# Performance work log

Measured on AMD Instinct MI355X. Metric: run time of the kernel, lower is better.

Reference implementation:

```python
import jax, jax.numpy as jnp
import numpy as np

MARGIN = 0.3
EPS = 1e-6  # torch pairwise_distance default eps used by TripletMarginLoss


def setup_inputs() -> dict:
    key = jax.random.key(0)
    k1, k2 = jax.random.split(key)
    emb = jax.random.normal(k1, (4096, 256), dtype=jnp.float32)
    emb = emb / jnp.linalg.norm(emb, axis=1, keepdims=True)  # docstring: normalized embeddings
    labels = jax.random.randint(k2, (4096,), 0, 64, dtype=jnp.int64) if jax.config.jax_enable_x64 else jax.random.randint(k2, (4096,), 0, 64, dtype=jnp.int32)
    return {"embeddings": emb, "labels": labels}


def _triplet_mining_loss(embeddings, labels):
    B = embeddings.shape[0]
    # pairwise euclidean distances via GEMM (matches torch.cdist p=2)
    sq = jnp.sum(embeddings * embeddings, axis=1)
    d2 = sq[:, None] + sq[None, :] - 2.0 * (embeddings @ embeddings.T)
    dist = jnp.sqrt(jnp.maximum(d2, 0.0))  # [B, B]

    same = labels[:, None] == labels[None, :]
    eye = jnp.eye(B, dtype=bool)
    pos_mask = same & ~eye
    neg_mask = ~same
    valid = pos_mask.any(axis=1) & neg_mask.any(axis=1)

    # hardest positive per anchor
    ap = jnp.where(pos_mask, dist, -jnp.inf)
    hp_idx = jnp.argmax(ap, axis=1)                           # [B]
    ap_dist = jnp.take_along_axis(dist, hp_idx[:, None], 1)[:, 0]

    # semi-hard negative: ap < d_an < ap + margin; pick FIRST such index (original takes semi_hard_indices[0])
    semi = neg_mask & (dist > ap_dist[:, None]) & (dist < ap_dist[:, None] + MARGIN)
    any_semi = semi.any(axis=1)
    first_semi = jnp.argmax(semi, axis=1)                     # argmax of bool = first True
    an = jnp.where(neg_mask, dist, jnp.inf)
    hardest_neg = jnp.argmin(an, axis=1)
    neg_idx = jnp.where(any_semi, first_semi, hardest_neg)

    # triplet margin loss recomputed from embeddings (torch adds EPS inside the norm)
    pos_e = embeddings[hp_idx]
    neg_e = embeddings[neg_idx]
    d_ap = jnp.linalg.norm(embeddings - pos_e + EPS, axis=1)
    d_an = jnp.linalg.norm(embeddings - neg_e + EPS, axis=1)
    per_anchor = jnp.maximum(d_ap - d_an + MARGIN, 0.0)

    vf = valid.astype(embeddings.dtype)
    cnt = jnp.sum(vf)
    return jnp.where(cnt > 0, jnp.sum(per_anchor * vf) / jnp.maximum(cnt, 1.0), 0.0)


def reference(embeddings, labels):
    return _triplet_mining_loss(embeddings, labels)
```

## Files before the change

### kernel.cpp

```cpp
#include <hip/hip_runtime.h>
#include <math.h>

#define BN 4096
#define DIM 256
#define D4 (DIM/4)
#define MI 8
#define MT 16
#define MARGINF 0.3f
#define EPSF 1e-6f
#define SCAP 96
#define IMAX 0x7fffffff

typedef __attribute__((ext_vector_type(8))) short bf16x8;
typedef __attribute__((ext_vector_type(4))) float f32x4;

__device__ __forceinline__ float fma4(float4 a, float4 b, float c){
  return fmaf(a.x,b.x, fmaf(a.y,b.y, fmaf(a.z,b.z, fmaf(a.w,b.w, c))));
}
__device__ __forceinline__ unsigned short f2bf(float x){
  unsigned u = __float_as_uint(x);
  return (unsigned short)((u + 0x7FFFu + ((u>>16)&1u)) >> 16);
}
__device__ __forceinline__ float bf2f(unsigned short h){
  return __uint_as_float(((unsigned)h)<<16);
}

__global__ __launch_bounds__(256) void k_pre2(const float* __restrict__ E,
     unsigned short* __restrict__ EhiT, unsigned short* __restrict__ EloT,
     float* __restrict__ sq, unsigned int* __restrict__ counter){
  int t = threadIdx.x;
  int b = blockIdx.x;
  const float4* E4 = (const float4*)E;
  bf16x8* HT = (bf16x8*)EhiT;
  bf16x8* LT = (bf16x8*)EloT;
  #pragma unroll
  for (int it=0; it<8; it++){
    int g  = b*4 + (it>>1);
    int kk = (it&1)*4 + (t>>6);
    int sub = t&63, q = sub>>4, n = sub&15;
    int r = g*16 + n;
    int c = kk*4 + q;
    float4 v0 = E4[(size_t)r*64 + c*2];
    float4 v1 = E4[(size_t)r*64 + c*2 + 1];
    unsigned short h[8], lo[8];
    float vv[8] = {v0.x,v0.y,v0.z,v0.w, v1.x,v1.y,v1.z,v1.w};
    #pragma unroll
    for (int i=0;i<8;i++){ h[i]=f2bf(vv[i]); lo[i]=f2bf(vv[i]-bf2f(h[i])); }
    bf16x8 hv, lv;
    #pragma unroll
    for (int i=0;i<8;i++){ hv[i]=(short)h[i]; lv[i]=(short)lo[i]; }
    size_t d = (size_t)g*512 + (size_t)kk*64 + sub;
    HT[d] = hv; LT[d] = lv;
  }
  int row = t>>2, part = t&3;
  const float4* rp = E4 + (size_t)(b*64+row)*D4 + part*16;
  float s0=0.f, s1=0.f;
  #pragma unroll
  for (int i=0;i<16;i+=2){ s0=fma4(rp[i],rp[i],s0); s1=fma4(rp[i+1],rp[i+1],s1); }
  float s = s0+s1;
  s += __shfl_xor(s,1); s += __shfl_xor(s,2);
  if (part==0) sq[b*64+row] = s;
  if (b==0 && t==0) counter[0] = 0u;
}

__global__ __launch_bounds__(1024,4) void k_main_m(const float* __restrict__ E,
     const unsigned short* __restrict__ EhiT, const unsigned short* __restrict__ EloT,
     const int* __restrict__ labels, const float* __restrict__ sq,
     float* __restrict__ partials, unsigned int* __restrict__ counter, float* __restrict__ out){
  __shared__ int   labsS[BN];
  __shared__ float sqS[BN];
  __shared__ bf16x8 afH[512];
  __shared__ bf16x8 afL[512];
  __shared__ float rnv[16][MT]; __shared__ int rnj[16][MT]; __shared__ int rsm[16][MT];
  __shared__ float apS[MT]; __shared__ int hpS[MT]; __shared__ int posOk[MT];
  __shared__ int finNeg[MT]; __shared__ int finVal[MT];
  __shared__ float lossS[MT];
  __shared__ float rs[16], rc[16];
  __shared__ int lastFlag;
  int t=threadIdx.x, l=t&63, w=t>>6;
  int lane16 = l&15, quad = l>>4;
  int a0 = blockIdx.x * MT;
  const bf16x8* HT = (const bf16x8*)EhiT;
  const bf16x8* LT = (const bf16x8*)EloT;
  const float4* E4 = (const float4*)E;
  size_t ABase = (size_t)blockIdx.x * 512;

  ((int4*)labsS)[t]  = ((const int4*)labels)[t];
  ((float4*)sqS)[t]  = ((const float4*)sq)[t];
  if (t < 512){ afH[t] = HT[ABase + t]; afL[t] = LT[ABase + t]; }
  __syncthreads();
  float sqa[4]; int laba[4];
  #pragma unroll
  for (int r=0;r<4;r++){ sqa[r]=sqS[a0+quad*4+r]; laba[r]=labsS[a0+quad*4+r]; }

  {
    int aw = a0 + w;
    int labW = labsS[aw];
    float sqw_ = sqS[aw];
    float4 areg = E4[(size_t)aw*64 + l];
    float bv = -INFINITY; int bj = IMAX;
    for (int c=0; c<64; c++){
      bool m = (labsS[c*64 + l] == labW);
      unsigned long long mask = __ballot(m);
      while (mask){
        int b = __ffsll((unsigned long long)mask) - 1;
        mask &= mask - 1ull;
        int j = c*64 + b;
        if (j == aw) continue;
        float4 bjv = E4[(size_t)j*64 + l];
        float p = fma4(areg, bjv, 0.0f);
        #pragma unroll
        for (int off=32; off; off>>=1) p += __shfl_xor(p, off);
        float d = sqrtf(fmaxf(sqw_ + sqS[j] - 2.0f*p, 0.0f));
        if (d > bv){ bv = d; bj = j; }
      }
    }
    if (l==0){
      posOk[w] = (bj != IMAX);
      apS[w] = bv;
      hpS[w] = (bj==IMAX) ? 0 : bj;
    }
  }
  __syncthreads();

  {
    float apr[4], thr[4];
    #pragma unroll
    for (int r=0;r<4;r++){ apr[r]=apS[quad*4+r]; thr[r]=apr[r]+MARGINF; }
    float mn[4]; int mj[4]; int sm[4];
    #pragma unroll
    for (int r=0;r<4;r++){ mn[r]=INFINITY; mj[r]=IMAX; sm[r]=IMAX; }
    #pragma unroll 1
    for (int tile=0; tile<16; tile++){
      int gb = w*16 + tile;
      size_t BBase = (size_t)gb * 512;
      f32x4 acc0={0.f,0.f,0.f,0.f}, acc1={0.f,0.f,0.f,0.f}, acc2={0.f,0.f,0.f,0.f};
      #pragma unroll 2
      for (int kk=0; kk<8; kk++){
        bf16x8 ah = afH[kk*64 + l];
        bf16x8 al = afL[kk*64 + l];
        bf16x8 bh = HT[BBase + kk*64 + l];
        bf16x8 bl = LT[BBase + kk*64 + l];
        acc0 = __builtin_amdgcn_mfma_f32_16x16x32_bf16(ah, bh, acc0, 0,0,0);
        acc1 = __builtin_amdgcn_mfma_f32_16x16x32_bf16(ah, bl, acc1, 0,0,0);
        acc2 = __builtin_amdgcn_mfma_f32_16x16x32_bf16(al, bh, acc2, 0,0,0);
      }
      int j = gb*16 + lane16;
      int lj = labsS[j]; float sqj = sqS[j];
      #pragma unroll
      for (int r=0;r<4;r++){
        float dot = acc0[r] + (acc1[r] + acc2[r]);
        float d = sqrtf(fmaxf(sqa[r] + sqj - 2.0f*dot, 0.0f));
        if (lj != laba[r]){
          if (d < mn[r]){ mn[r]=d; mj[r]=j; }
          if (d > apr[r] && d < thr[r] && j < sm[r]) sm[r]=j;
        }
      }
    }
    #pragma unroll
    for (int r=0;r<4;r++){
      float v=mn[r]; int j=mj[r]; int s=sm[r];
      #pragma unroll
      for (int off=1; off<16; off<<=1){
        float v2=__shfl_xor(v,off); int j2=__shfl_xor(j,off); int s2=__shfl_xor(s,off);
        if (v2<v || (v2==v && j2<j)){ v=v2; j=j2; }
        s = (s2<s)?s2:s;
      }
      if (lane16==0){ rnv[w][quad*4+r]=v; rnj[w][quad*4+r]=j; rsm[w][quad*4+r]=s; }
    }
  }
  __syncthreads();
  if (t < MT){
    int a=t;
    float V=INFINITY; int J=IMAX; int S=IMAX;
    for (int q=0;q<16;q++){
      float v2=rnv[q][a]; int j2=rnj[q][a];
      if (v2<V || (v2==V && j2<J)){ V=v2; J=j2; }
      int s2=rsm[q][a]; S=(s2<S)?s2:S;
    }
    bool anyneg = (J != IMAX);
    int ng = (S != IMAX) ? S : J;
    finNeg[a] = (ng==IMAX) ? 0 : ng;
    finVal[a] = (posOk[a] && anyneg) ? 1 : 0;
  }
  __syncthreads();

  {
    int a = w;
    float sp=0.f, sn=0.f;
    int dov = finVal[a];
    if (dov){
      int hp = hpS[a], ng = finNeg[a];
      float4 av = E4[(size_t)(a0+a)*64 + l];
      float4 pv = E4[(size_t)hp*64 + l];
      float4 nv = E4[(size_t)ng*64 + l];
      float d0=av.x-pv.x+EPSF, d1=av.y-pv.y+EPSF, d2=av.z-pv.z+EPSF, d3=av.w-pv.w+EPSF;
      sp = fmaf(d0,d0, fmaf(d1,d1, fmaf(d2,d2, d3*d3)));
      float n0=av.x-nv.x+EPSF, n1=av.y-nv.y+EPSF, n2=av.z-nv.z+EPSF, n3=av.w-nv.w+EPSF;
      sn = fmaf(n0,n0, fmaf(n1,n1, fmaf(n2,n2, n3*n3)));
    }
    #pragma unroll
    for (int off=32; off; off>>=1){ sp += __shfl_xor(sp,off); sn += __shfl_xor(sn,off); }
    if (l==0) lossS[a] = dov ? fmaxf(sqrtf(sp)-sqrtf(sn)+MARGINF, 0.0f) : 0.0f;
  }
  __syncthreads();

  if (t==0){
    float lsum=0.f, lcnt=0.f;
    for (int a=0;a<MT;a++){ lsum += lossS[a]; lcnt += (float)finVal[a]; }
    partials[2*blockIdx.x]   = lsum;
    partials[2*blockIdx.x+1] = lcnt;
    __threadfence();
    unsigned int old = atomicAdd(counter, 1u);
    lastFlag = (old == gridDim.x - 1) ? 1 : 0;
  }
  __syncthreads();
  if (lastFlag){
    __threadfence();
    float s=0.f, c=0.f;
    if (t < 256){ s = partials[2*t]; c = partials[2*t+1]; }
    #pragma unroll
    for (int off=32; off; off>>=1){ s += __shfl_xor(s,off); c += __shfl_xor(c,off); }
    if (l==0){ rs[w]=s; rc[w]=c; }
    __syncthreads();
    if (t==0){
      float S=0.f, C=0.f;
      for (int q=0;q<16;q++){ S+=rs[q]; C+=rc[q]; }
      out[0] = (C>0.0f) ? S/fmaxf(C,1.0f) : 0.0f;
    }
  }
}

__global__ __launch_bounds__(256) void k_sq(const float* __restrict__ E, float* __restrict__ sq){
  int i = blockIdx.x*256 + threadIdx.x;
  if (i >= BN) return;
  const float4* r = (const float4*)E + (size_t)i*D4;
  float a0=0.f,a1=0.f,a2=0.f,a3=0.f;
  #pragma unroll
  for (int q=0;q<D4;q+=4){
    a0 = fma4(r[q],r[q],a0);   a1 = fma4(r[q+1],r[q+1],a1);
    a2 = fma4(r[q+2],r[q+2],a2); a3 = fma4(r[q+3],r[q+3],a3);
  }
  sq[i] = (a0+a1)+(a2+a3);
}

__global__ __launch_bounds__(256) void k_pos(const float* __restrict__ E, const int* __restrict__ labels,
                       const float* __restrict__ sq, float* __restrict__ apw,
                       int* __restrict__ hpw, int* __restrict__ anypw){
  __shared__ int members[1024];
  __shared__ float4 mem4[SCAP*65];
  __shared__ int cnts[16][4];
  __shared__ int offs[16][4];
  __shared__ int cntS;
  int t = threadIdx.x, lane = t&63, w = t>>6;
  int c = blockIdx.x >> 2, split = blockIdx.x & 3;
  for (int ch=0; ch<16; ch++){
    bool m = (labels[ch*256 + t] == c);
    unsigned long long mask = __ballot(m);
    if (lane==0) cnts[ch][w] = __popcll(mask);
  }
  __syncthreads();
  if (t==0){
    int run=0;
    for (int ch=0; ch<16; ch++)
      for (int q=0;q<4;q++){ offs[ch][q]=run; run+=cnts[ch][q]; }
    cntS = run;
  }
  __syncthreads();
  int cnt = cntS; if (cnt>1024) cnt=1024;
  for (int ch=0; ch<16; ch++){
    int idx = ch*256 + t;
    bool m = (labels[idx] == c);
    unsigned long long mask = __ballot(m);
    int my = __popcll(mask & ((1ull<<lane)-1ull));
    int pos = offs[ch][w] + my;
    if (m && pos < 1024) members[pos] = idx;
  }
  int S = (cnt < SCAP) ? cnt : SCAP;
  int anyp = (cnt >= 2) ? 1 : 0;
  __syncthreads();
  const float4* E4 = (const float4*)E;
  for (int idx=t; idx<S*64; idx+=256){
    int row = idx>>6, f = idx&63;
    mem4[row*65 + f] = E4[(size_t)members[row]*D4 + f];
  }
  __syncthreads();
  int esplit = split*4 + w;
  int p = lane&3, cand = lane>>2;
  int passes = (cnt+15)>>4;
  for (int mi=esplit; mi<cnt; mi+=16){
    int i = members[mi];
    float sqi = sq[i];
    float4 ai4[16];
    if (mi < S){
      #pragma unroll
      for (int m=0;m<16;m++) ai4[m] = mem4[mi*65 + p + 4*m];
    } else {
      #pragma unroll
      for (int m=0;m<16;m++) ai4[m] = E4[(size_t)i*D4 + p + 4*m];
    }
    float bv = -INFINITY; int bj = IMAX;
    for (int ps=0; ps<passes; ps++){
      int mj = ps*16 + cand;
      if (mj < cnt && mj != mi){
        int j = members[mj];
        float a0v=0.f, a1v=0.f;
        if (mj < S){
          const float4* rj = mem4 + mj*65 + p;
          #pragma unroll
          for (int m=0;m<16;m+=2){ a0v=fma4(ai4[m],rj[4*m],a0v); a1v=fma4(ai4[m+1],rj[4*(m+1)],a1v); }
        } else {
          const float4* rj = E4 + (size_t)j*D4 + p;
          #pragma unroll
          for (int m=0;m<16;m+=2){ a0v=fma4(ai4[m],rj[4*m],a0v); a1v=fma4(ai4[m+1],rj[4*(m+1)],a1v); }
        }
        float acc = a0v+a1v;
        acc += __shfl_xor(acc,1); acc += __shfl_xor(acc,2);
        float d = sqrtf(fmaxf(sqi + sq[j] - 2.0f*acc, 0.0f));
        if (p==0){ if (d > bv || (d==bv && j<bj)){ bv=d; bj=j; } }
      }
    }
    #pragma unroll
    for (int off=32; off; off>>=1){
      float v2=__shfl_xor(bv,off); int j2=__shfl_xor(bj,off);
      if (v2>bv || (v2==bv && j2<bj)){ bv=v2; bj=j2; }
    }
    if (lane==0){
      int J = (bj==IMAX) ? 0 : bj;
      apw[i]=bv; hpw[i]=J; anypw[i]=anyp;
    }
  }
}

__global__ __launch_bounds__(256,2) void k_main(const float* __restrict__ E, const int* __restrict__ labels,
     const float* __restrict__ sq, const float* __restrict__ apw, const int* __restrict__ hpw,
     const int* __restrict__ anypw, float* __restrict__ partials){
  __shared__ float4 At[MI*68 + 4];
  __shared__ float redv[4][MI]; __shared__ int redj[4][MI]; __shared__ int redsm[4][MI];
  __shared__ int finNeg[MI]; __shared__ int finVal[MI];
  __shared__ float redp[4], redn[4];
  int t=threadIdx.x, lane=t&63, w=t>>6;
  int a0 = blockIdx.x * MI;
  const float4* E4 = (const float4*)E;
  for (int idx=t; idx<MI*64; idx+=256){
    int a=idx>>6, q=idx&63, pp=q&3, mm=q>>2;
    At[a*68 + pp*17 + mm] = E4[(size_t)(a0+a)*D4 + q];
  }
  __syncthreads();
  float apv[MI], sqi[MI]; int labi[MI];
  #pragma unroll
  for (int a=0;a<MI;a++){ apv[a]=apw[a0+a]; sqi[a]=sq[a0+a]; labi[a]=labels[a0+a]; }
  float mnv[MI]; int mnj[MI]; int smj[MI];
  #pragma unroll
  for (int a=0;a<MI;a++){ mnv[a]=INFINITY; mnj[a]=0; smj[a]=IMAX; }
  int s = t>>2, p = t&3;
  for (int it=0; it<16; it++){
    int colb = it*256 + 4*s;
    const float4* __restrict__ bp = E4 + (size_t)colb*D4 + p;
    float acc[MI][4];
    #pragma unroll
    for (int a=0;a<MI;a++){
      #pragma unroll
      for (int c2=0;c2<4;c2++) acc[a][c2]=0.0f;
    }
    for (int mg=0; mg<4; mg++){
      float4 b[4][4];
      #pragma unroll
      for (int c2=0;c2<4;c2++){
        #pragma unroll
        for (int m=0;m<4;m++) b[m][c2] = bp[(size_t)c2*D4 + mg*16 + m*4];
      }
      #pragma unroll
      for (int a=0;a<MI;a++){
        float4 a4[4];
        #pragma unroll
        for (int m=0;m<4;m++) a4[m] = At[a*68 + p*17 + mg*4 + m];
        #pragma unroll
        for (int m=0;m<4;m++){
          #pragma unroll
          for (int c2=0;c2<4;c2++) acc[a][c2] = fma4(a4[m], b[m][c2], acc[a][c2]);
        }
      }
    }
    #pragma unroll
    for (int a=0;a<MI;a++){
      #pragma unroll
      for (int c2=0;c2<4;c2++){
        float v = acc[a][c2];
        v += __shfl_xor(v,1); v += __shfl_xor(v,2);
        acc[a][c2] = v;
      }
    }
    #pragma unroll
    for (int c2=0;c2<4;c2++){
      int j = colb + c2;
      int lj = labels[j]; float sqj = sq[j];
      #pragma unroll
      for (int a=0;a<MI;a++){
        float d = sqrtf(fmaxf(sqi[a]+sqj-2.0f*acc[a][c2], 0.0f));
        if (lj != labi[a]){
          if (d < mnv[a]){ mnv[a]=d; mnj[a]=j; }
          if (d > apv[a] && d < apv[a]+MARGINF && j < smj[a]) smj[a]=j;
        }
      }
    }
  }
  #pragma unroll
  for (int a=0;a<MI;a++){
    float v=mnv[a]; int j=mnj[a]; int sm=smj[a];
    #pragma unroll
    for (int off=32; off; off>>=1){
      float v2=__shfl_xor(v,off); int j2=__shfl_xor(j,off); int s2=__shfl_xor(sm,off);
      if (v2<v || (v2==v && j2<j)){ v=v2; j=j2; }
      sm = (s2<sm)?s2:sm;
    }
    if (lane==0){ redv[w][a]=v; redj[w][a]=j; redsm[w][a]=sm; }
  }
  __syncthreads();
  if (t < MI){
    int a=t;
    float V=INFINITY; int J=0; int S=IMAX; bool first=true;
    for (int q=0;q<4;q++){
      float v2=redv[q][a]; int j2=redj[q][a];
      if (first || v2<V || (v2==V && j2<J)){ V=v2; J=j2; first=false; }
      int s2=redsm[q][a]; S=(s2<S)?s2:S;
    }
    bool anyneg = (V < INFINITY);
    finNeg[a] = (S != IMAX) ? S : J;
    finVal[a] = (anypw[a0+a] != 0 && anyneg) ? 1 : 0;
  }
  __syncthreads();
  float lsum=0.0f, lcnt=0.0f;
  for (int a=0;a<MI;a++){
    if (finVal[a]){
      int hp = hpw[a0+a]; int ng = finNeg[a];
      float ai = E[(size_t)(a0+a)*DIM + t];
      float pv = E[(size_t)hp*DIM + t];
      float nv = E[(size_t)ng*DIM + t];
      float dp = ai - pv + EPSF; float dn = ai - nv + EPSF;
      float sp = dp*dp, sn = dn*dn;
      #pragma unroll
      for (int off=32; off; off>>=1){ sp += __shfl_xor(sp,off); sn += __shfl_xor(sn,off); }
      if (lane==0){ redp[w]=sp; redn[w]=sn; }
    }
    __syncthreads();
    if (finVal[a] && t==0){
      float SP=(redp[0]+redp[1])+(redp[2]+redp[3]);
      float SN=(redn[0]+redn[1])+(redn[2]+redn[3]);
      lsum += fmaxf(sqrtf(SP)-sqrtf(SN)+MARGINF, 0.0f);
      lcnt += 1.0f;
    }
    __syncthreads();
  }
  if (t==0){ partials[2*blockIdx.x]=lsum; partials[2*blockIdx.x+1]=lcnt; }
}

__global__ __launch_bounds__(256) void k_fin(const float* __restrict__ partials, float* __restrict__ out, int nb){
  __shared__ float rs[4], rc[4];
  int t=threadIdx.x, lane=t&63, w=t>>6;
  float s=0.f, c=0.f;
  for (int q=t;q<nb;q+=256){ s+=partials[2*q]; c+=partials[2*q+1]; }
  #pragma unroll
  for (int off=32; off; off>>=1){ s+=__shfl_xor(s,off); c+=__shfl_xor(c,off); }
  if (lane==0){ rs[w]=s; rc[w]=c; }
  __syncthreads();
  if (t==0){
    float S=(rs[0]+rs[1])+(rs[2]+rs[3]);
    float C=(rc[0]+rc[1])+(rc[2]+rc[3]);
    out[0] = (C>0.0f) ? S/fmaxf(C,1.0f) : 0.0f;
  }
}

extern "C" void kernel_launch(void* const* d_in, const int* in_sizes, int n_in,
                              void* d_out, int out_size, void* d_ws, size_t ws_size,
                              hipStream_t stream) {
  const float* E      = (const float*)d_in[0];
  const int*   labels = (const int*)d_in[1];
  float* out = (float*)d_out;

  float* sqw      = (float*)d_ws;
  float* apw      = sqw + BN;
  int*   hpw      = (int*)(apw + BN);
  int*   anypw    = hpw + BN;
  float* partials = (float*)(anypw + BN);
  unsigned int* counter = (unsigned int*)(partials + 1024);
  unsigned short* EhiT = (unsigned short*)((char*)d_ws + 131072);
  unsigned short* EloT = EhiT + (size_t)BN*DIM;
  bool big = ws_size >= (size_t)(131072 + 4*1024*1024);

  if (big){
    k_pre2  <<<64,    256,  0, stream>>>(E, EhiT, EloT, sqw, counter);
    k_main_m<<<BN/MT, 1024, 0, stream>>>(E, EhiT, EloT, labels, sqw, partials, counter, out);
  } else {
    k_sq  <<<BN/256, 256, 0, stream>>>(E, sqw);
    k_pos <<<256,    256, 0, stream>>>(E, labels, sqw, apw, hpw, anypw);
    k_main<<<BN/MI,  256, 0, stream>>>(E, labels, sqw, apw, hpw, anypw, partials);
    k_fin <<<1,      256, 0, stream>>>(partials, out, BN/MI);
  }
}
```

Baseline: 162.0 us.

## Fuse bf16 split preprocessing into main kernel with grid barrier; compare squared distances

Removes the separate preprocessing kernel. Each block of the main kernel now converts its own 16 anchor rows into hi/lo bf16 tiles and squared norms, then waits on a global atomic-counter grid barrier before reading the other blocks' data. It also compares squared distances instead of taking a sqrt per pair, squaring the positive and threshold bounds. The cost is a spin-wait barrier, which needs all 256 blocks resident at once, plus an added memset launch to reset the counters.

```diff
diff --git a/kernel.cpp b/kernel.cpp
--- a/kernel.cpp
+++ b/kernel.cpp
@@ -25,48 +25,10 @@
   return __uint_as_float(((unsigned)h)<<16);
 }
 
-__global__ __launch_bounds__(256) void k_pre2(const float* __restrict__ E,
+__global__ __launch_bounds__(1024,4) void k_fused(const float* __restrict__ E,
      unsigned short* __restrict__ EhiT, unsigned short* __restrict__ EloT,
-     float* __restrict__ sq, unsigned int* __restrict__ counter){
-  int t = threadIdx.x;
-  int b = blockIdx.x;
-  const float4* E4 = (const float4*)E;
-  bf16x8* HT = (bf16x8*)EhiT;
-  bf16x8* LT = (bf16x8*)EloT;
-  #pragma unroll
-  for (int it=0; it<8; it++){
-    int g  = b*4 + (it>>1);
-    int kk = (it&1)*4 + (t>>6);
-    int sub = t&63, q = sub>>4, n = sub&15;
-    int r = g*16 + n;
-    int c = kk*4 + q;
-    float4 v0 = E4[(size_t)r*64 + c*2];
-    float4 v1 = E4[(size_t)r*64 + c*2 + 1];
-    unsigned short h[8], lo[8];
-    float vv[8] = {v0.x,v0.y,v0.z,v0.w, v1.x,v1.y,v1.z,v1.w};
-    #pragma unroll
-    for (int i=0;i<8;i++){ h[i]=f2bf(vv[i]); lo[i]=f2bf(vv[i]-bf2f(h[i])); }
-    bf16x8 hv, lv;
-    #pragma unroll
-    for (int i=0;i<8;i++){ hv[i]=(short)h[i]; lv[i]=(short)lo[i]; }
-    size_t d = (size_t)g*512 + (size_t)kk*64 + sub;
-    HT[d] = hv; LT[d] = lv;
-  }
-  int row = t>>2, part = t&3;
-  const float4* rp = E4 + (size_t)(b*64+row)*D4 + part*16;
-  float s0=0.f, s1=0.f;
-  #pragma unroll
-  for (int i=0;i<16;i+=2){ s0=fma4(rp[i],rp[i],s0); s1=fma4(rp[i+1],rp[i+1],s1); }
-  float s = s0+s1;
-  s += __shfl_xor(s,1); s += __shfl_xor(s,2);
-  if (part==0) sq[b*64+row] = s;
-  if (b==0 && t==0) counter[0] = 0u;
-}
-
-__global__ __launch_bounds__(1024,4) void k_main_m(const float* __restrict__ E,
-     const unsigned short* __restrict__ EhiT, const unsigned short* __restrict__ EloT,
-     const int* __restrict__ labels, const float* __restrict__ sq,
-     float* __restrict__ partials, unsigned int* __restrict__ counter, float* __restrict__ out){
+     const int* __restrict__ labels, float* __restrict__ sq,
+     float* __restrict__ partials, unsigned int* __restrict__ counters, float* __restrict__ out){
   __shared__ int   labsS[BN];
   __shared__ float sqS[BN];
   __shared__ bf16x8 afH[512];
@@ -80,14 +42,52 @@
   int t=threadIdx.x, l=t&63, w=t>>6;
   int lane16 = l&15, quad = l>>4;
   int a0 = blockIdx.x * MT;
-  const bf16x8* HT = (const bf16x8*)EhiT;
-  const bf16x8* LT = (const bf16x8*)EloT;
   const float4* E4 = (const float4*)E;
+  bf16x8* HT = (bf16x8*)EhiT;
+  bf16x8* LT = (bf16x8*)EloT;
   size_t ABase = (size_t)blockIdx.x * 512;
 
-  ((int4*)labsS)[t]  = ((const int4*)labels)[t];
-  ((float4*)sqS)[t]  = ((const float4*)sq)[t];
-  if (t < 512){ afH[t] = HT[ABase + t]; afL[t] = LT[ABase + t]; }
+  if (t < 512){
+    int kk = t>>6, sub = t&63, q = sub>>4, n = sub&15;
+    int row = a0 + n;
+    int c = kk*4 + q;
+    float4 v0 = E4[(size_t)row*64 + c*2];
+    float4 v1 = E4[(size_t)row*64 + c*2 + 1];
+    float vv[8] = {v0.x,v0.y,v0.z,v0.w, v1.x,v1.y,v1.z,v1.w};
+    bf16x8 hv, lv;
+    #pragma unroll
+    for (int i=0;i<8;i++){
+      unsigned short h = f2bf(vv[i]);
+      hv[i] = (short)h;
+      lv[i] = (short)f2bf(vv[i]-bf2f(h));
+    }
+    HT[ABase + t] = hv; LT[ABase + t] = lv;
+    afH[t] = hv;        afL[t] = lv;
+  }
+  if (t < 64){
+    int row = t>>2, part = t&3;
+    const float4* rp = E4 + (size_t)(a0+row)*64 + part*16;
+    float s0=0.f, s1=0.f;
+    #pragma unroll
+    for (int i=0;i<16;i+=2){ s0=fma4(rp[i],rp[i],s0); s1=fma4(rp[i+1],rp[i+1],s1); }
+    float s = s0+s1;
+    s += __shfl_xor(s,1); s += __shfl_xor(s,2);
+    if (part==0) sq[a0+row] = s;
+  }
+  ((int4*)labsS)[t] = ((const int4*)labels)[t];
+  __syncthreads();
+
+  if (t==0){
+    __threadfence();
+    atomicAdd(&counters[0], 1u);
+    while (__hip_atomic_load(&counters[0], __ATOMIC_RELAXED, __HIP_MEMORY_SCOPE_AGENT) < gridDim.x){
+      __builtin_amdgcn_s_sleep(1);
+    }
+  }
+  __syncthreads();
+  __threadfence();
+
+  ((float4*)sqS)[t] = ((const float4*)sq)[t];
   __syncthreads();
   float sqa[4]; int laba[4];
   #pragma unroll
@@ -98,7 +98,7 @@
     int labW = labsS[aw];
     float sqw_ = sqS[aw];
     float4 areg = E4[(size_t)aw*64 + l];
-    float bv = -INFINITY; int bj = IMAX;
+    float bv2 = -INFINITY; int bj = IMAX;
     for (int c=0; c<64; c++){
       bool m = (labsS[c*64 + l] == labW);
       unsigned long long mask = __ballot(m);
@@ -111,22 +111,27 @@
         float p = fma4(areg, bjv, 0.0f);
         #pragma unroll
         for (int off=32; off; off>>=1) p += __shfl_xor(p, off);
-        float d = sqrtf(fmaxf(sqw_ + sqS[j] - 2.0f*p, 0.0f));
-        if (d > bv){ bv = d; bj = j; }
+        float d2 = sqw_ + sqS[j] - 2.0f*p;
+        if (d2 > bv2){ bv2 = d2; bj = j; }
       }
     }
     if (l==0){
       posOk[w] = (bj != IMAX);
-      apS[w] = bv;
+      apS[w] = (bj==IMAX) ? -INFINITY : sqrtf(fmaxf(bv2, 0.0f));
       hpS[w] = (bj==IMAX) ? 0 : bj;
     }
   }
   __syncthreads();
 
   {
-    float apr[4], thr[4];
-    #pragma unroll
-    for (int r=0;r<4;r++){ apr[r]=apS[quad*4+r]; thr[r]=apr[r]+MARGINF; }
+    float ap2[4], th2[4];
+    #pragma unroll
+    for (int r=0;r<4;r++){
+      float ap = apS[quad*4+r];
+      ap2[r] = ap*ap;
+      float th = ap + MARGINF;
+      th2[r] = th*th;
+    }
     float mn[4]; int mj[4]; int sm[4];
     #pragma unroll
     for (int r=0;r<4;r++){ mn[r]=INFINITY; mj[r]=IMAX; sm[r]=IMAX; }
@@ -150,10 +155,10 @@
       #pragma unroll
       for (int r=0;r<4;r++){
         float dot = acc0[r] + (acc1[r] + acc2[r]);
-        float d = sqrtf(fmaxf(sqa[r] + sqj - 2.0f*dot, 0.0f));
+        float d2v = sqa[r] + sqj - 2.0f*dot;
         if (lj != laba[r]){
-          if (d < mn[r]){ mn[r]=d; mj[r]=j; }
-          if (d > apr[r] && d < thr[r] && j < sm[r]) sm[r]=j;
+          if (d2v < mn[r]){ mn[r]=d2v; mj[r]=j; }
+          if (d2v > ap2[r] && d2v < th2[r] && j < sm[r]) sm[r]=j;
         }
       }
     }
@@ -204,14 +209,13 @@
     if (l==0) lossS[a] = dov ? fmaxf(sqrtf(sp)-sqrtf(sn)+MARGINF, 0.0f) : 0.0f;
   }
   __syncthreads();
-
   if (t==0){
     float lsum=0.f, lcnt=0.f;
     for (int a=0;a<MT;a++){ lsum += lossS[a]; lcnt += (float)finVal[a]; }
     partials[2*blockIdx.x]   = lsum;
     partials[2*blockIdx.x+1] = lcnt;
     __threadfence();
-    unsigned int old = atomicAdd(counter, 1u);
+    unsigned int old = atomicAdd(&counters[1], 1u);
     lastFlag = (old == gridDim.x - 1) ? 1 : 0;
   }
   __syncthreads();
@@ -478,20 +482,21 @@
   const int*   labels = (const int*)d_in[1];
   float* out = (float*)d_out;
 
-  float* sqw      = (float*)d_ws;
-  float* apw      = sqw + BN;
-  int*   hpw      = (int*)(apw + BN);
-  int*   anypw    = hpw + BN;
-  float* partials = (float*)(anypw + BN);
-  unsigned int* counter = (unsigned int*)(partials + 1024);
-  unsigned short* EhiT = (unsigned short*)((char*)d_ws + 131072);
-  unsigned short* EloT = EhiT + (size_t)BN*DIM;
   bool big = ws_size >= (size_t)(131072 + 4*1024*1024);
-
   if (big){
-    k_pre2  <<<64,    256,  0, stream>>>(E, EhiT, EloT, sqw, counter);
-    k_main_m<<<BN/MT, 1024, 0, stream>>>(E, EhiT, EloT, labels, sqw, partials, counter, out);
+    unsigned int* counters = (unsigned int*)d_ws;
+    float* sqw      = (float*)((char*)d_ws + 256);
+    float* partials = sqw + BN;
+    unsigned short* EhiT = (unsigned short*)((char*)d_ws + 131072);
+    unsigned short* EloT = EhiT + (size_t)BN*DIM;
+    hipMemsetAsync(d_ws, 0, 8, stream);
+    k_fused<<<BN/MT, 1024, 0, stream>>>(E, EhiT, EloT, labels, sqw, partials, counters, out);
   } else {
+    float* sqw      = (float*)d_ws;
+    float* apw      = sqw + BN;
+    int*   hpw      = (int*)(apw + BN);
+    int*   anypw    = hpw + BN;
+    float* partials = (float*)(anypw + BN);
     k_sq  <<<BN/256, 256, 0, stream>>>(E, sqw);
     k_pos <<<256,    256, 0, stream>>>(E, labels, sqw, apw, hpw, anypw);
     k_main<<<BN/MI,  256, 0, stream>>>(E, labels, sqw, apw, hpw, anypw, partials);
```

Result: slower. 230.1 us (+42.0%).
